# Kernel tuning notes

Hardware: AMD Instinct MI355X
Metric: run time of the kernel (lower is better)

## Reference

```python
import jax, jax.numpy as jnp
import numpy as np

N_HEADS = 16
D_MODEL = 1024
D_HEAD = D_MODEL // N_HEADS


def setup_inputs() -> dict:
    key = jax.random.key(0)
    ks = jax.random.split(key, 5)
    scale = 0.02
    x = jax.random.normal(ks[0], (2, 2048, D_MODEL), dtype=jnp.float32)
    # torch.nn.Linear weights: (out_features, in_features)
    w_in = jax.random.normal(ks[1], (3 * D_MODEL, D_MODEL), dtype=jnp.float32) * scale
    b_in = jax.random.normal(ks[2], (3 * D_MODEL,), dtype=jnp.float32) * scale
    w_out = jax.random.normal(ks[3], (D_MODEL, D_MODEL), dtype=jnp.float32) * scale
    b_out = jax.random.normal(ks[4], (D_MODEL,), dtype=jnp.float32) * scale
    return {"x": x, "w_in": w_in, "b_in": b_in, "w_out": w_out, "b_out": b_out}


def reference(x, w_in, b_in, w_out, b_out):
    B, S, D = x.shape
    H, Dh = N_HEADS, D_HEAD
    qkv = x @ w_in.T + b_in                      # [B,S,3D]
    q, k, v = jnp.split(qkv, 3, axis=-1)
    q = q.reshape(B, S, H, Dh).transpose(0, 2, 1, 3)  # [B,H,S,Dh]
    k = k.reshape(B, S, H, Dh).transpose(0, 2, 1, 3)
    v = v.reshape(B, S, H, Dh).transpose(0, 2, 1, 3)
    scores = jnp.einsum('bhqd,bhkd->bhqk', q, k) / jnp.sqrt(jnp.float32(Dh))
    weights = jax.nn.softmax(scores, axis=-1)
    out = jnp.einsum('bhqk,bhkd->bhqd', weights, v)   # [B,H,S,Dh]
    # Faithful to original: reshape WITHOUT transposing heads back
    out = out.reshape(B, S, D)
    return out @ w_out.T + b_out
```

## Files before the change

### kernel.cpp

```cpp
#include <hip/hip_runtime.h>
#include <math.h>

constexpr int D_MODEL = 1024;
constexpr int N_HEADS = 16;
constexpr int D_HEAD  = 64;
constexpr int SEQ     = 2048;
constexpr int BATCH   = 2;
constexpr int M_ROWS  = BATCH * SEQ;
constexpr int QKV_N   = 3 * D_MODEL;
constexpr int KDIM    = 1024;
constexpr int NROWS   = BATCH * N_HEADS * SEQ;

typedef __bf16 bf16x8 __attribute__((ext_vector_type(8)));
typedef float  f32x4  __attribute__((ext_vector_type(4)));
typedef float  f32x16 __attribute__((ext_vector_type(16)));
typedef unsigned uint2v __attribute__((ext_vector_type(2)));

union U4 { uint4 u; bf16x8 b; ushort s[8]; };
union U2 { uint2 u; ushort s[4]; };

__device__ __forceinline__ unsigned pk2bf(float lo, float hi) {
    union { unsigned u; __bf16 b[2]; } cv;
    cv.b[0] = (__bf16)lo; cv.b[1] = (__bf16)hi;
    return cv.u;
}
__device__ __forceinline__ ushort f2bf(float f) {
    union { ushort s[2]; __bf16 b[2]; } cv;
    cv.b[0] = (__bf16)f;
    return cv.s[0];
}

__device__ __forceinline__ int swz(int row, int bytecol) {
    return row * 128 + (bytecol ^ ((row & 7) << 4));
}

__device__ __forceinline__ void gload16(const void* g, void* l) {
    __builtin_amdgcn_global_load_lds(
        (const __attribute__((address_space(1))) unsigned int*)g,
        (__attribute__((address_space(3))) unsigned int*)l, 16, 0, 0);
}

#define QSCALE 0.18033688011112042f

__device__ __forceinline__ void pack_paf(const f32x16& s, bf16x8& f0o, bf16x8& f1o) {
    const unsigned q0 = pk2bf(s[0],  s[1]);
    const unsigned q1 = pk2bf(s[2],  s[3]);
    const unsigned q2 = pk2bf(s[4],  s[5]);
    const unsigned q3 = pk2bf(s[6],  s[7]);
    const unsigned q4 = pk2bf(s[8],  s[9]);
    const unsigned q5 = pk2bf(s[10], s[11]);
    const unsigned q6 = pk2bf(s[12], s[13]);
    const unsigned q7 = pk2bf(s[14], s[15]);
    const uint2v x = __builtin_amdgcn_permlane32_swap(q0, q2, false, false);
    const uint2v y = __builtin_amdgcn_permlane32_swap(q1, q3, false, false);
    const uint2v z = __builtin_amdgcn_permlane32_swap(q4, q6, false, false);
    const uint2v u = __builtin_amdgcn_permlane32_swap(q5, q7, false, false);
    U4 f0; f0.u.x = x[0]; f0.u.y = y[0]; f0.u.z = x[1]; f0.u.w = y[1];
    U4 f1; f1.u.x = z[0]; f1.u.y = u[0]; f1.u.z = z[1]; f1.u.w = u[1];
    f0o = f0.b; f1o = f1.b;
}

__global__ __launch_bounds__(256)
void convert3_kernel(const float* __restrict__ x,  ushort* __restrict__ xo,
                     const float* __restrict__ wi, ushort* __restrict__ wio,
                     const float* __restrict__ wo, ushort* __restrict__ woo) {
    const int na = M_ROWS * D_MODEL;
    const int nb = QKV_N * D_MODEL;
    const int nc = D_MODEL * D_MODEL;
    const int total = (na + nb + nc) / 8;
    for (int g = blockIdx.x * blockDim.x + threadIdx.x; g < total;
         g += gridDim.x * blockDim.x) {
        const int i = g * 8;
        const float* src; ushort* dst; int off;
        if (i < na)           { src = x;  dst = xo;  off = i; }
        else if (i < na + nb) { src = wi; dst = wio; off = i - na; }
        else                  { src = wo; dst = woo; off = i - na - nb; }
        const float4 a = *reinterpret_cast<const float4*>(src + off);
        const float4 b = *reinterpret_cast<const float4*>(src + off + 4);
        uint4 o;
        o.x = pk2bf(a.x, a.y); o.y = pk2bf(a.z, a.w);
        o.z = pk2bf(b.x, b.y); o.w = pk2bf(b.z, b.w);
        *reinterpret_cast<uint4*>(dst + off) = o;
    }
}

__device__ __forceinline__ void mfma_gemm_bt_128_2ph(
    const ushort* __restrict__ Ag, const ushort* __restrict__ Bg,
    int m0, int n0, ushort (*As)[128 * 32], ushort (*Bs)[128 * 32],
    f32x4 (&acc)[4][4])
{
    const int tid = threadIdx.x;
    const int l   = tid & 63;
    const int rl  = l & 15, hh = l >> 4;
    const int w   = tid >> 6;
    const int wm  = (w >> 1) * 64, wn = (w & 1) * 64;

    const int r0 = tid >> 2;
    const int ce = (tid & 3) * 8;
    const ushort* gA0 = Ag + (size_t)(m0 + r0) * KDIM + ce;
    const ushort* gA1 = gA0 + (size_t)64 * KDIM;
    const ushort* gB0 = Bg + (size_t)(n0 + r0) * KDIM + ce;
    const ushort* gB1 = gB0 + (size_t)64 * KDIM;
    const int lo = tid * 16;

    gload16(gA0, (char*)As[0] + lo);
    gload16(gA1, (char*)As[0] + lo + 4096);
    gload16(gB0, (char*)Bs[0] + lo);
    gload16(gB1, (char*)Bs[0] + lo + 4096);
    __syncthreads();

    int cur = 0;
    for (int k0 = 0; k0 < KDIM; k0 += 32) {
        if (k0 + 32 < KDIM) {
            gload16(gA0 + k0 + 32, (char*)As[cur ^ 1] + lo);
            gload16(gA1 + k0 + 32, (char*)As[cur ^ 1] + lo + 4096);
            gload16(gB0 + k0 + 32, (char*)Bs[cur ^ 1] + lo);
            gload16(gB1 + k0 + 32, (char*)Bs[cur ^ 1] + lo + 4096);
        }
        bf16x8 af[4], bf_[4];
        #pragma unroll
        for (int f = 0; f < 4; ++f)
            af[f]  = *(const bf16x8*)((const char*)As[cur] + (wm + f * 16 + rl) * 64 + hh * 16);
        #pragma unroll
        for (int f = 0; f < 4; ++f)
            bf_[f] = *(const bf16x8*)((const char*)Bs[cur] + (wn + f * 16 + rl) * 64 + hh * 16);
        #pragma unroll
        for (int i = 0; i < 4; ++i)
            #pragma unroll
            for (int j = 0; j < 4; ++j)
                acc[i][j] = __builtin_amdgcn_mfma_f32_16x16x32_bf16(af[i], bf_[j], acc[i][j], 0, 0, 0);
        __syncthreads();
        cur ^= 1;
    }
}

__global__ __launch_bounds__(256)
void qkv_mfma_kernel(const ushort* __restrict__ xb, const ushort* __restrict__ wb,
                     const float* __restrict__ b_in,
                     ushort* __restrict__ Q, ushort* __restrict__ K, ushort* __restrict__ V) {
    __shared__ __align__(16) ushort As[2][128 * 32];
    __shared__ __align__(16) ushort Bs[2][128 * 32];

    f32x4 acc[4][4];
    #pragma unroll
    for (int i = 0; i < 4; ++i)
        #pragma unroll
        for (int j = 0; j < 4; ++j) acc[i][j] = (f32x4){0.f, 0.f, 0.f, 0.f};

    const int m0 = blockIdx.y * 128, n0 = blockIdx.x * 128;
    mfma_gemm_bt_128_2ph(xb, wb, m0, n0, As, Bs, acc);

    const int l  = threadIdx.x & 63, w = threadIdx.x >> 6;
    const int rl = l & 15, hh = l >> 4;
    const int mb = m0 + (w >> 1) * 64, nb = n0 + (w & 1) * 64;

    #pragma unroll
    for (int j = 0; j < 4; ++j) {
        const int n  = nb + j * 16 + rl;
        const float bias = b_in[n];
        const int t  = n >> 10;
        const int jj = n & 1023;
        const int h  = jj >> 6;
        const int d  = jj & 63;
        ushort* dst = (t == 0) ? Q : (t == 1) ? K : V;
        const float sc = (t == 0) ? QSCALE : 1.0f;
        #pragma unroll
        for (int i = 0; i < 4; ++i)
            #pragma unroll
            for (int r = 0; r < 4; ++r) {
                const int m = mb + i * 16 + hh * 4 + r;
                const int b = m >> 11;
                const int s = m & (SEQ - 1);
                dst[((size_t)(b * N_HEADS + h) * SEQ + s) * D_HEAD + d] =
                    f2bf((acc[i][j][r] + bias) * sc);
            }
    }
}

__global__ __launch_bounds__(512)
void attn_mfma_split_kernel(const ushort* __restrict__ Q, const ushort* __restrict__ K,
                            const ushort* __restrict__ V, ushort* __restrict__ Op,
                            float* __restrict__ lbuf) {
    __shared__ __align__(16) char Ks[2][64 * 128];
    __shared__ __align__(16) char Vs[2][64 * 128];

    const int tid = threadIdx.x;
    const int w   = tid >> 6;
    const int l   = tid & 63;
    const int l31 = l & 31;
    const int lh  = l >> 5;

    const int bid  = blockIdx.x;
    const int nid  = (bid & 7) * 64 + (bid >> 3);
    const int bh   = nid >> 4;
    const int rem  = nid & 15;
    const int half = rem >> 3;
    const int qt   = rem & 7;

    const size_t base  = (size_t)bh * SEQ * D_HEAD;
    const size_t kbase = base + (size_t)half * 1024 * D_HEAD;
    const int qbase = qt * 256 + w * 32;

    bf16x8 qf[4];
    {
        const ushort* qp = Q + base + (size_t)(qbase + l31) * D_HEAD + lh * 8;
        #pragma unroll
        for (int c = 0; c < 4; ++c) {
            U4 t; t.u = *(const uint4*)(qp + c * 16);
            qf[c] = t.b;
        }
    }

    f32x16 ot0, ot1;
    #pragma unroll
    for (int r = 0; r < 16; ++r) { ot0[r] = 0.f; ot1[r] = 0.f; }
    float l_run = 0.0f;

    const int sr  = tid >> 3, seg = tid & 7;
    const int kp  = (tid & 31) * 2, dc = (tid >> 5) * 4;
    const ushort* gK  = K + kbase + (size_t)sr * D_HEAD + seg * 8;
    const ushort* gV0 = V + kbase + (size_t)kp * D_HEAD + dc;
    const ushort* gV1 = gV0 + D_HEAD;

    uint4 ka; U2 va, vb;
    ka   = *(const uint4*)(gK);
    va.u = *(const uint2*)(gV0);
    vb.u = *(const uint2*)(gV1);
    {
        char* kd = Ks[0]; char* vd = Vs[0];
        *(uint4*)(kd + swz(sr, seg * 16)) = ka;
        #pragma unroll
        for (int i = 0; i < 4; ++i) {
            const int d = dc + i;
            *(unsigned*)(vd + d * 128 + ((kp * 2) ^ ((d & 7) << 4))) =
                (unsigned)va.s[i] | ((unsigned)vb.s[i] << 16);
        }
    }

    constexpr int NT = 1024 / 64;
    for (int t = 0; t < NT; ++t) {
        const int cur = t & 1;
        __syncthreads();

        if (t + 1 < NT) {
            const size_t off = (size_t)(t + 1) * 64 * D_HEAD;
            ka   = *(const uint4*)(gK + off);
            va.u = *(const uint2*)(gV0 + off);
            vb.u = *(const uint2*)(gV1 + off);
        }
        const char* kbuf = Ks[cur];
        const char* vbuf = Vs[cur];

        f32x16 st0, st1;
        #pragma unroll
        for (int r = 0; r < 16; ++r) { st0[r] = 0.f; st1[r] = 0.f; }
        #pragma unroll
        for (int c = 0; c < 4; ++c) {
            const bf16x8 kf0 = *(const bf16x8*)(kbuf + swz(l31,      c * 32 + lh * 16));
            st0 = __builtin_amdgcn_mfma_f32_32x32x16_bf16(kf0, qf[c], st0, 0, 0, 0);
            const bf16x8 kf1 = *(const bf16x8*)(kbuf + swz(32 + l31, c * 32 + lh * 16));
            st1 = __builtin_amdgcn_mfma_f32_32x32x16_bf16(kf1, qf[c], st1, 0, 0, 0);
        }

        float pa = 0.f, pb = 0.f, pc = 0.f, pd = 0.f;
        #pragma unroll
        for (int r = 0; r < 8; ++r) {
            st0[r]     = __builtin_amdgcn_exp2f(st0[r]);     pa += st0[r];
            st0[8 + r] = __builtin_amdgcn_exp2f(st0[8 + r]); pb += st0[8 + r];
            st1[r]     = __builtin_amdgcn_exp2f(st1[r]);     pc += st1[r];
            st1[8 + r] = __builtin_amdgcn_exp2f(st1[8 + r]); pd += st1[8 + r];
        }
        l_run += (pa + pb) + (pc + pd);

        bf16x8 paf[4];
        pack_paf(st0, paf[0], paf[1]);
        pack_paf(st1, paf[2], paf[3]);

        #pragma unroll
        for (int kc = 0; kc < 4; ++kc) {
            const bf16x8 vf0 = *(const bf16x8*)(vbuf + swz(l31,      kc * 32 + lh * 16));
            ot0 = __builtin_amdgcn_mfma_f32_32x32x16_bf16(vf0, paf[kc], ot0, 0, 0, 0);
            const bf16x8 vf1 = *(const bf16x8*)(vbuf + swz(32 + l31, kc * 32 + lh * 16));
            ot1 = __builtin_amdgcn_mfma_f32_32x32x16_bf16(vf1, paf[kc], ot1, 0, 0, 0);
        }

        if (t + 1 < NT) {
            char* kd = Ks[cur ^ 1]; char* vd = Vs[cur ^ 1];
            *(uint4*)(kd + swz(sr, seg * 16)) = ka;
            #pragma unroll
            for (int i = 0; i < 4; ++i) {
                const int d = dc + i;
                *(unsigned*)(vd + d * 128 + ((kp * 2) ^ ((d & 7) << 4))) =
                    (unsigned)va.s[i] | ((unsigned)vb.s[i] << 16);
            }
        }
    }

    l_run += __shfl_xor(l_run, 32, 64);
    const size_t grow = (size_t)bh * SEQ + qbase + l31;
    ushort* op = Op + ((size_t)half * NROWS + grow) * D_HEAD;
    #pragma unroll
    for (int dt = 0; dt < 2; ++dt) {
        const f32x16& o = dt ? ot1 : ot0;
        #pragma unroll
        for (int g = 0; g < 4; ++g) {
            const int d0 = dt * 32 + g * 8 + lh * 4;
            uint2 s2;
            s2.x = pk2bf(o[g * 4 + 0], o[g * 4 + 1]);
            s2.y = pk2bf(o[g * 4 + 2], o[g * 4 + 3]);
            *(uint2*)(op + d0) = s2;
        }
    }
    if (lh == 0) lbuf[(size_t)half * NROWS + grow] = l_run;
}

__global__ __launch_bounds__(256)
void combine_kernel(const ushort* __restrict__ Op, const float* __restrict__ lbuf,
                    ushort* __restrict__ A) {
    const int idx = blockIdx.x * 256 + threadIdx.x;
    const int row = idx >> 3;
    const int dc  = (idx & 7) * 8;
    const float inv = 1.0f / (lbuf[row] + lbuf[NROWS + row]);
    U4 o1, o2;
    o1.u = *(const uint4*)(Op + (size_t)row * D_HEAD + dc);
    o2.u = *(const uint4*)(Op + ((size_t)NROWS + row) * D_HEAD + dc);
    uint4 r;
    float v[8];
    #pragma unroll
    for (int i = 0; i < 8; ++i)
        v[i] = ((float)o1.b[i] + (float)o2.b[i]) * inv;
    r.x = pk2bf(v[0], v[1]); r.y = pk2bf(v[2], v[3]);
    r.z = pk2bf(v[4], v[5]); r.w = pk2bf(v[6], v[7]);
    *(uint4*)(A + (size_t)row * D_HEAD + dc) = r;
}

__global__ __launch_bounds__(256)
void out_mfma_kernel(const ushort* __restrict__ Ab, const ushort* __restrict__ wb,
                     const float* __restrict__ b_out, float* __restrict__ out) {
    __shared__ __align__(16) ushort As[2][128 * 32];
    __shared__ __align__(16) ushort Bs[2][128 * 32];

    f32x4 acc[4][4];
    #pragma unroll
    for (int i = 0; i < 4; ++i)
        #pragma unroll
        for (int j = 0; j < 4; ++j) acc[i][j] = (f32x4){0.f, 0.f, 0.f, 0.f};

    const int m0 = blockIdx.y * 128, n0 = blockIdx.x * 128;
    mfma_gemm_bt_128_2ph(Ab, wb, m0, n0, As, Bs, acc);

    const int l  = threadIdx.x & 63, w = threadIdx.x >> 6;
    const int rl = l & 15, hh = l >> 4;
    const int mb = m0 + (w >> 1) * 64, nb = n0 + (w & 1) * 64;

    #pragma unroll
    for (int j = 0; j < 4; ++j) {
        const int n = nb + j * 16 + rl;
        const float bias = b_out[n];
        #pragma unroll
        for (int i = 0; i < 4; ++i)
            #pragma unroll
            for (int r = 0; r < 4; ++r) {
                const int m = mb + i * 16 + hh * 4 + r;
                out[(size_t)m * D_MODEL + n] = acc[i][j][r] + bias;
            }
    }
}

extern "C" void kernel_launch(void* const* d_in, const int* in_sizes, int n_in,
                              void* d_out, int out_size, void* d_ws, size_t ws_size,
                              hipStream_t stream) {
    const float* x     = (const float*)d_in[0];
    const float* w_in  = (const float*)d_in[1];
    const float* b_in  = (const float*)d_in[2];
    const float* w_out = (const float*)d_in[3];
    const float* b_out = (const float*)d_in[4];
    float* out = (float*)d_out;

    const size_t T = (size_t)BATCH * N_HEADS * SEQ * D_HEAD;
    ushort* Qw  = (ushort*)d_ws;
    ushort* Kw  = Qw + T;
    ushort* Vw  = Kw + T;
    ushort* Opw = Vw + T;
    ushort* xb  = Opw + T;
    ushort* wib = xb + T;
    ushort* wob = wib + (size_t)QKV_N * D_MODEL;
    float*  lw  = (float*)(wob + (size_t)D_MODEL * D_MODEL);
    ushort* Aw  = Qw;

    convert3_kernel<<<2048, 256, 0, stream>>>(x, xb, w_in, wib, w_out, wob);

    qkv_mfma_kernel<<<dim3(QKV_N / 128, M_ROWS / 128), 256, 0, stream>>>(
        xb, wib, b_in, Qw, Kw, Vw);
    attn_mfma_split_kernel<<<512, 512, 0, stream>>>(Qw, Kw, Vw, Opw, lw);
    combine_kernel<<<NROWS * 8 / 256, 256, 0, stream>>>(Opw, lw, Aw);
    out_mfma_kernel<<<dim3(D_MODEL / 128, M_ROWS / 128), 256, 0, stream>>>(
        Aw, wob, b_out, out);
}
```

Measured before the change: 120.1 us.

## Fuse split-attention combine into attention kernel via atomic completion flags

```diff
diff --git a/kernel.cpp b/kernel.cpp
--- a/kernel.cpp
+++ b/kernel.cpp
@@ -63,7 +63,9 @@
 __global__ __launch_bounds__(256)
 void convert3_kernel(const float* __restrict__ x,  ushort* __restrict__ xo,
                      const float* __restrict__ wi, ushort* __restrict__ wio,
-                     const float* __restrict__ wo, ushort* __restrict__ woo) {
+                     const float* __restrict__ wo, ushort* __restrict__ woo,
+                     int* __restrict__ flags) {
+    if (blockIdx.x == 0 && threadIdx.x < 256) flags[threadIdx.x] = 0;
     const int na = M_ROWS * D_MODEL;
     const int nb = QKV_N * D_MODEL;
     const int nc = D_MODEL * D_MODEL;
@@ -180,9 +182,11 @@
 __global__ __launch_bounds__(512)
 void attn_mfma_split_kernel(const ushort* __restrict__ Q, const ushort* __restrict__ K,
                             const ushort* __restrict__ V, ushort* __restrict__ Op,
-                            float* __restrict__ lbuf) {
+                            float* __restrict__ lbuf, ushort* __restrict__ A,
+                            int* __restrict__ flags) {
     __shared__ __align__(16) char Ks[2][64 * 128];
     __shared__ __align__(16) char Vs[2][64 * 128];
+    __shared__ int role_sh;
 
     const int tid = threadIdx.x;
     const int w   = tid >> 6;
@@ -312,26 +316,35 @@
         }
     }
     if (lh == 0) lbuf[(size_t)half * NROWS + grow] = l_run;
-}
-
-__global__ __launch_bounds__(256)
-void combine_kernel(const ushort* __restrict__ Op, const float* __restrict__ lbuf,
-                    ushort* __restrict__ A) {
-    const int idx = blockIdx.x * 256 + threadIdx.x;
-    const int row = idx >> 3;
-    const int dc  = (idx & 7) * 8;
-    const float inv = 1.0f / (lbuf[row] + lbuf[NROWS + row]);
-    U4 o1, o2;
-    o1.u = *(const uint4*)(Op + (size_t)row * D_HEAD + dc);
-    o2.u = *(const uint4*)(Op + ((size_t)NROWS + row) * D_HEAD + dc);
-    uint4 r;
-    float v[8];
-    #pragma unroll
-    for (int i = 0; i < 8; ++i)
-        v[i] = ((float)o1.b[i] + (float)o2.b[i]) * inv;
-    r.x = pk2bf(v[0], v[1]); r.y = pk2bf(v[2], v[3]);
-    r.z = pk2bf(v[4], v[5]); r.w = pk2bf(v[6], v[7]);
-    *(uint4*)(A + (size_t)row * D_HEAD + dc) = r;
+
+    __threadfence();
+    __syncthreads();
+    if (tid == 0) role_sh = atomicAdd(&flags[bh * 8 + qt], 1);
+    __syncthreads();
+    if (role_sh == 1) {
+        __threadfence();
+        const int sh = half ^ 1;
+        const float lsib = lbuf[(size_t)sh * NROWS + grow];
+        const float inv  = 1.0f / (l_run + lsib);
+        const ushort* so = Op + ((size_t)sh * NROWS + grow) * D_HEAD;
+        ushort* ap = A + grow * D_HEAD;
+        #pragma unroll
+        for (int dt = 0; dt < 2; ++dt) {
+            #pragma unroll
+            for (int g = 0; g < 4; ++g) {
+                const int d0 = dt * 32 + g * 8 + lh * 4;
+                union { uint2 u; __bf16 b[4]; } a1, a2;
+                a1.u = *(const uint2*)(op + d0);
+                a2.u = *(const uint2*)(so + d0);
+                uint2 r;
+                r.x = pk2bf(((float)a1.b[0] + (float)a2.b[0]) * inv,
+                            ((float)a1.b[1] + (float)a2.b[1]) * inv);
+                r.y = pk2bf(((float)a1.b[2] + (float)a2.b[2]) * inv,
+                            ((float)a1.b[3] + (float)a2.b[3]) * inv);
+                *(uint2*)(ap + d0) = r;
+            }
+        }
+    }
 }
 
 __global__ __launch_bounds__(256)
@@ -386,14 +399,14 @@
     ushort* wib = xb + T;
     ushort* wob = wib + (size_t)QKV_N * D_MODEL;
     float*  lw  = (float*)(wob + (size_t)D_MODEL * D_MODEL);
+    int*    flags = (int*)(lw + 2 * (size_t)NROWS);
     ushort* Aw  = Qw;
 
-    convert3_kernel<<<2048, 256, 0, stream>>>(x, xb, w_in, wib, w_out, wob);
+    convert3_kernel<<<2048, 256, 0, stream>>>(x, xb, w_in, wib, w_out, wob, flags);
 
     qkv_mfma_kernel<<<dim3(QKV_N / 128, M_ROWS / 128), 256, 0, stream>>>(
         xb, wib, b_in, Qw, Kw, Vw);
-    attn_mfma_split_kernel<<<512, 512, 0, stream>>>(Qw, Kw, Vw, Opw, lw);
-    combine_kernel<<<NROWS * 8 / 256, 256, 0, stream>>>(Opw, lw, Aw);
+    attn_mfma_split_kernel<<<512, 512, 0, stream>>>(Qw, Kw, Vw, Opw, lw, Aw, flags);
     out_mfma_kernel<<<dim3(D_MODEL / 128, M_ROWS / 128), 256, 0, stream>>>(
         Aw, wob, b_out, out);
 }
```

Measured after the change: 323.4 us. +169.3%, slower.
